# Kernel optimization log

Measured on AMD Instinct MI355X. Metric: run time of the kernel, lower is better.

Reference implementation:

```python
import jax, jax.numpy as jnp
import numpy as np

EPS = 1e-5  # torch LayerNorm default eps
ALIBI_SLOPE = 1.0

def layer_norm(x, g, b):
    mu = x.mean(-1, keepdims=True)
    var = ((x - mu) ** 2).mean(-1, keepdims=True)
    return (x - mu) * jax.lax.rsqrt(var + EPS) * g + b

def setup_inputs() -> dict:
    key = jax.random.key(0)
    B, T, D, DK, F = 4, 4096, 1024, 128, 2048  # F = ffn_mult * d_model
    ks = jax.random.split(key, 6)
    def s(k, shp, fan):
        return jax.random.normal(k, shp, jnp.float32) / np.sqrt(fan).astype(np.float32)
    return {
        'x': jax.random.normal(ks[0], (B, T, D), jnp.float32),
        'ln1_g': jnp.ones((D,), jnp.float32), 'ln1_b': jnp.zeros((D,), jnp.float32),
        'Wq': s(ks[1], (DK, D), D),  # torch Linear weight layout (out, in)
        'Wk': s(ks[2], (DK, D), D),
        'Wv': s(ks[3], (D, D), D),
        'ln2_g': jnp.ones((D,), jnp.float32), 'ln2_b': jnp.zeros((D,), jnp.float32),
        'W1': s(ks[4], (F, D), D), 'b1': jnp.zeros((F,), jnp.float32),
        'W2': s(ks[5], (D, F), F), 'b2': jnp.zeros((D,), jnp.float32),
    }

def reference(x, ln1_g, ln1_b, Wq, Wk, Wv, ln2_g, ln2_b, W1, b1, W2, b2):
    B, T, D = x.shape
    dk = Wq.shape[0]
    h = layer_norm(x, ln1_g, ln1_b)
    q = jnp.einsum('btd,kd->btk', h, Wq)
    k = jnp.einsum('btd,kd->btk', h, Wk)
    att = jnp.einsum('btk,bsk->bts', q, k) * (dk ** -0.5)  # [B,T,T]
    pos = jnp.arange(T)
    dist = jnp.clip(pos[:, None] - pos[None, :], 0).astype(att.dtype)
    att = att - ALIBI_SLOPE * dist  # alibi bias
    causal = pos[:, None] >= pos[None, :]
    att = jnp.where(causal, att, -jnp.inf)
    att = jax.nn.softmax(att, axis=-1)
    ctx = jnp.einsum('bts,bsd->btd', att, h)  # note: attends over h, not a v-projection
    x = x + jnp.einsum('btd,ed->bte', ctx, Wv)
    h2 = layer_norm(x, ln2_g, ln2_b)
    ff = jnp.maximum(jnp.einsum('btd,fd->btf', h2, W1) + b1, 0.0)
    x = x + jnp.einsum('btf,df->btd', ff, W2) + b2
    return x
```

## Files before the change

kernel.cpp:

```cpp
#include <hip/hip_runtime.h>
#include <stdint.h>

typedef __attribute__((ext_vector_type(4))) float f32x4;
typedef __attribute__((ext_vector_type(8))) unsigned short u16x8;
typedef __attribute__((ext_vector_type(4))) unsigned short u16x4;
typedef unsigned short bf16_t;

#define DEV __device__ __forceinline__

DEV void mfma16(f32x4& d, u16x8 a, u16x8 b) {
    asm("v_mfma_f32_16x16x32_bf16 %0, %1, %2, %0" : "+v"(d) : "v"(a), "v"(b));
}

DEV bf16_t f2bf(float f) {
    uint32_t u = __builtin_bit_cast(uint32_t, f);
    return (bf16_t)((u + 0x7fffu + ((u >> 16) & 1u)) >> 16);
}

DEV void async_g2l16(const void* g, void* l) {
    __builtin_amdgcn_global_load_lds(
        (const __attribute__((address_space(1))) uint32_t*)(uintptr_t)g,
        (__attribute__((address_space(3))) uint32_t*)(uint32_t)(uintptr_t)l,
        16, 0, 0);
}

DEV void blockbar() {
    asm volatile("" ::: "memory");
    __builtin_amdgcn_s_barrier();
    asm volatile("" ::: "memory");
}

#define VMCNT(n) asm volatile("s_waitcnt vmcnt(" #n ")" ::: "memory")

template <int EPI>
__global__ __launch_bounds__(512, 4) void gemm256x128_nt(
    const bf16_t* __restrict__ A, const bf16_t* __restrict__ B,
    void* __restrict__ Cp, const float* __restrict__ bias,
    const float* __restrict__ res, int M, int N, int K)
{
    __shared__ bf16_t sA[2 * 8192];
    __shared__ bf16_t sB[2 * 4096];
    const int tid = threadIdx.x;
    const int wave = tid >> 6, lane = tid & 63;
    const int lcol = lane & 15, krow = lane >> 4;
    const int wm = wave >> 1, wn = wave & 1;

    int id  = blockIdx.y * gridDim.x + blockIdx.x;
    int nwg = gridDim.x * gridDim.y;
    int swz = ((nwg & 7) == 0) ? ((id & 7) * (nwg >> 3) + (id >> 3)) : id;
    const int bn = swz % gridDim.y;
    const int bm = swz / gridDim.y;
    const int row_a = bm * 256, col_c = bn * 128;

    const int tq = tid >> 2;
    const int tr = (((tid & 3) ^ ((tid >> 3) & 3)) * 8);
    const bf16_t* aSt = A + (size_t)(row_a + tq) * K + tr;
    const bf16_t* bSt = B + (size_t)(col_c + tq) * K + tr;
    const size_t rowstep = (size_t)128 * K;
    bf16_t* ldsAw = sA + wave * 512;
    bf16_t* ldsBw = sB + wave * 512;

    const int cswz = (krow ^ ((lcol >> 1) & 3)) * 8;
    const int raOff = (wm * 64 + lcol) * 32 + cswz;
    const int rbOff = (wn * 64 + lcol) * 32 + cswz;

    f32x4 acc[4][4] = {};
    const int nt = K >> 5;

    async_g2l16(aSt,           ldsAw);
    async_g2l16(aSt + rowstep, ldsAw + 4096);
    async_g2l16(bSt,           ldsBw);
    VMCNT(0);
    blockbar();

    for (int t = 0; t < nt; ++t) {
        const int ra = (t & 1) ? 8192 : 0;
        const int rb = (t & 1) ? 4096 : 0;
        const int wa = 8192 - ra, wb = 4096 - rb;
        const bool pf = (t + 1) < nt;
        const size_t ko = (size_t)(t + 1) * 32;
        u16x8 fa[4], fb[4];
#pragma unroll
        for (int i = 0; i < 4; i++) fa[i] = *(const u16x8*)&sA[ra + raOff + i * 512];
#pragma unroll
        for (int i = 0; i < 4; i++) fb[i] = *(const u16x8*)&sB[rb + rbOff + i * 512];
        if (pf) {
            async_g2l16(aSt + ko,           ldsAw + wa);
            async_g2l16(aSt + ko + rowstep, ldsAw + wa + 4096);
            async_g2l16(bSt + ko,           ldsBw + wb);
        }
        __builtin_amdgcn_s_setprio(1);
#pragma unroll
        for (int mi = 0; mi < 4; mi++)
#pragma unroll
            for (int ni = 0; ni < 4; ni++)
                mfma16(acc[mi][ni], fa[mi], fb[ni]);
        __builtin_amdgcn_s_setprio(0);
        VMCNT(0);
        blockbar();
    }

#pragma unroll
    for (int mi = 0; mi < 4; mi++)
#pragma unroll
        for (int ni = 0; ni < 4; ni++)
#pragma unroll
            for (int j = 0; j < 4; j++) {
                const int gr = row_a + wm * 64 + mi * 16 + krow * 4 + j;
                const int gc = col_c + wn * 64 + ni * 16 + lcol;
                float v = acc[mi][ni][j];
                if (EPI == 0) {
                    ((bf16_t*)Cp)[(size_t)gr * N + gc] = f2bf(v);
                } else if (EPI == 1) {
                    v += bias[gc];
                    v = fmaxf(v, 0.f);
                    ((bf16_t*)Cp)[(size_t)gr * N + gc] = f2bf(v);
                } else if (EPI == 2) {
                    ((float*)Cp)[(size_t)gr * N + gc] = v + res[(size_t)gr * N + gc];
                } else {
                    ((float*)Cp)[(size_t)gr * N + gc] = v + bias[gc] + res[(size_t)gr * N + gc];
                }
            }
}

template <int EPI>
__global__ __launch_bounds__(256) void gemm_nt(
    const bf16_t* __restrict__ A, const bf16_t* __restrict__ B,
    void* __restrict__ Cp, const float* __restrict__ bias,
    const float* __restrict__ res, int M, int N, int K)
{
    alignas(16) __shared__ bf16_t sA[128 * 32];
    alignas(16) __shared__ bf16_t sB[128 * 32];
    const int tid = threadIdx.x;
    const int wave = tid >> 6, lane = tid & 63;
    const int lcol = lane & 15, krow = lane >> 4;

    int id  = blockIdx.y * gridDim.x + blockIdx.x;
    int nwg = gridDim.x * gridDim.y;
    int swz = ((nwg & 7) == 0) ? ((id & 7) * (nwg >> 3) + (id >> 3)) : id;
    const int bn = swz % gridDim.y;
    const int bm = swz / gridDim.y;

    const int row_a = bm * 128, col_c = bn * 128;
    const int wm = (wave >> 1) * 64, wn = (wave & 1) * 64;

    const int   srow  = wave * 16 + (lane >> 2);
    const int   scol  = (lane & 3) * 8;
    const bf16_t* aSrc = A + (size_t)(row_a + srow) * K + scol;
    const bf16_t* bSrc = B + (size_t)(col_c + srow) * K + scol;
    char* sAl = (char*)sA + wave * 1024;
    char* sBl = (char*)sB + wave * 1024;
    const size_t rstep = (size_t)64 * K;

    f32x4 acc[4][4] = {};

    for (int k0 = 0; k0 < K; k0 += 32) {
        async_g2l16(aSrc + k0,         sAl);
        async_g2l16(aSrc + k0 + rstep, sAl + 4096);
        async_g2l16(bSrc + k0,         sBl);
        async_g2l16(bSrc + k0 + rstep, sBl + 4096);
        __syncthreads();
        u16x8 af[4], bfr[4];
#pragma unroll
        for (int i = 0; i < 4; i++) {
            af[i]  = *(const u16x8*)&sA[(wm + i * 16 + lcol) * 32 + krow * 8];
            bfr[i] = *(const u16x8*)&sB[(wn + i * 16 + lcol) * 32 + krow * 8];
        }
#pragma unroll
        for (int mi = 0; mi < 4; mi++)
#pragma unroll
            for (int ni = 0; ni < 4; ni++)
                mfma16(acc[mi][ni], af[mi], bfr[ni]);
        __syncthreads();
    }

#pragma unroll
    for (int mi = 0; mi < 4; mi++)
#pragma unroll
        for (int ni = 0; ni < 4; ni++)
#pragma unroll
            for (int j = 0; j < 4; j++) {
                const int gr = row_a + wm + mi * 16 + krow * 4 + j;
                const int gc = col_c + wn + ni * 16 + lcol;
                float v = acc[mi][ni][j];
                if (EPI == 0) {
                    ((bf16_t*)Cp)[(size_t)gr * N + gc] = f2bf(v);
                } else if (EPI == 1) {
                    v += bias[gc];
                    v = fmaxf(v, 0.f);
                    ((bf16_t*)Cp)[(size_t)gr * N + gc] = f2bf(v);
                } else if (EPI == 2) {
                    ((float*)Cp)[(size_t)gr * N + gc] = v + res[(size_t)gr * N + gc];
                } else {
                    ((float*)Cp)[(size_t)gr * N + gc] = v + bias[gc] + res[(size_t)gr * N + gc];
                }
            }
}

__global__ __launch_bounds__(256) void ln_kernel(
    const float* __restrict__ X, const float* __restrict__ G,
    const float* __restrict__ Bt, bf16_t* __restrict__ O)
{
    const int row = blockIdx.x, tid = threadIdx.x;
    const int wave = tid >> 6, lane = tid & 63;
    const size_t base = (size_t)row * 1024 + tid * 4;
    f32x4 xv = *(const f32x4*)&X[base];
    float s  = xv[0] + xv[1] + xv[2] + xv[3];
    float s2 = xv[0]*xv[0] + xv[1]*xv[1] + xv[2]*xv[2] + xv[3]*xv[3];
#pragma unroll
    for (int o = 1; o < 64; o <<= 1) { s += __shfl_xor(s, o); s2 += __shfl_xor(s2, o); }
    __shared__ float red[8];
    if (lane == 0) { red[wave] = s; red[wave + 4] = s2; }
    __syncthreads();
    s  = red[0] + red[1] + red[2] + red[3];
    s2 = red[4] + red[5] + red[6] + red[7];
    const float mu = s * (1.f / 1024.f);
    const float rs = rsqrtf(s2 * (1.f / 1024.f) - mu * mu + 1e-5f);
    f32x4 gv = *(const f32x4*)&G[tid * 4];
    f32x4 bv = *(const f32x4*)&Bt[tid * 4];
    u16x4 ov;
#pragma unroll
    for (int i = 0; i < 4; i++) ov[i] = f2bf((xv[i] - mu) * rs * gv[i] + bv[i]);
    *(u16x4*)&O[base] = ov;
}

__global__ __launch_bounds__(256) void cvt_f32_bf16(
    const float* __restrict__ src, bf16_t* __restrict__ dst, int n)
{
    int i = (blockIdx.x * 256 + threadIdx.x) * 4;
    if (i >= n) return;
    f32x4 v = *(const f32x4*)&src[i];
    u16x4 o;
#pragma unroll
    for (int t = 0; t < 4; t++) o[t] = f2bf(v[t]);
    *(u16x4*)&dst[i] = o;
}

__global__ __launch_bounds__(256) void attn_p(
    const bf16_t* __restrict__ QK, bf16_t* __restrict__ P, int T)
{
    const int tid = threadIdx.x, w = tid >> 6, lane = tid & 63;
    const int lcol = lane & 15, krow = lane >> 4;
    const int qt = blockIdx.x;
    const int ntb = T >> 6;
    const int b = qt / ntb;
    const int r0 = (qt - b * ntb) << 6;
    const size_t g0 = (size_t)b * T + r0;
    const int jbase = r0 - 192;
    const float scale = 0.08838834764831845f;

    __shared__ float lred[2][4][64];

    u16x8 qf[4][4];
#pragma unroll
    for (int mf = 0; mf < 4; mf++)
#pragma unroll
        for (int ks = 0; ks < 4; ks++)
            qf[mf][ks] = *(const u16x8*)&QK[(g0 + mf * 16 + lcol) * 256 + ks * 32 + krow * 8];

    f32x4 acc[4][4] = {};
    const size_t kbase = (size_t)b * T * 256 + 128;
#pragma unroll
    for (int ks = 0; ks < 4; ks++) {
        u16x8 kf[4];
#pragma unroll
        for (int nf = 0; nf < 4; nf++) {
            int jc = jbase + w * 64 + nf * 16 + lcol;
            int jr = jc < 0 ? 0 : jc;
            kf[nf] = *(const u16x8*)&QK[kbase + (size_t)jr * 256 + ks * 32 + krow * 8];
        }
#pragma unroll
        for (int mf = 0; mf < 4; mf++)
#pragma unroll
            for (int nf = 0; nf < 4; nf++)
                mfma16(acc[mf][nf], qf[mf][ks], kf[nf]);
    }

#pragma unroll
    for (int mf = 0; mf < 4; mf++)
#pragma unroll
        for (int j = 0; j < 4; j++) {
            const int i_ = r0 + mf * 16 + krow * 4 + j;
            float m = -1e30f;
#pragma unroll
            for (int nf = 0; nf < 4; nf++) {
                const int jc = jbase + w * 64 + nf * 16 + lcol;
                float sv = (jc >= 0 && jc <= i_) ? acc[mf][nf][j] * scale - (float)(i_ - jc) : -1e30f;
                acc[mf][nf][j] = sv;
                m = fmaxf(m, sv);
            }
#pragma unroll
            for (int o = 1; o < 16; o <<= 1) m = fmaxf(m, __shfl_xor(m, o));
            if (lcol == 0) lred[0][w][mf * 16 + krow * 4 + j] = m;
        }
    __syncthreads();

#pragma unroll
    for (int mf = 0; mf < 4; mf++)
#pragma unroll
        for (int j = 0; j < 4; j++) {
            const int rr = mf * 16 + krow * 4 + j;
            const float m = fmaxf(fmaxf(lred[0][0][rr], lred[0][1][rr]),
                                  fmaxf(lred[0][2][rr], lred[0][3][rr]));
            float sm = 0.f;
#pragma unroll
            for (int nf = 0; nf < 4; nf++) {
                float p = __expf(acc[mf][nf][j] - m);
                acc[mf][nf][j] = p;
                sm += p;
            }
#pragma unroll
            for (int o = 1; o < 16; o <<= 1) sm += __shfl_xor(sm, o);
            if (lcol == 0) lred[1][w][rr] = sm;
        }
    __syncthreads();

    float inv_l[4][4];
#pragma unroll
    for (int mf = 0; mf < 4; mf++)
#pragma unroll
        for (int j = 0; j < 4; j++) {
            const int rr = mf * 16 + krow * 4 + j;
            inv_l[mf][j] = 1.f / (lred[1][0][rr] + lred[1][1][rr] + lred[1][2][rr] + lred[1][3][rr]);
        }
#pragma unroll
    for (int mf = 0; mf < 4; mf++)
#pragma unroll
        for (int nf = 0; nf < 4; nf++)
#pragma unroll
            for (int j = 0; j < 4; j++) {
                const int rr = mf * 16 + krow * 4 + j;
                P[((size_t)qt * 64 + rr) * 256 + w * 64 + nf * 16 + lcol] =
                    f2bf(acc[mf][nf][j] * inv_l[mf][j]);
            }
}

__global__ __launch_bounds__(256) void pv_gemm(
    const bf16_t* __restrict__ P, const bf16_t* __restrict__ H,
    bf16_t* __restrict__ CTX, int T)
{
    alignas(16) __shared__ bf16_t sHt[128 * 40];
    const int tid = threadIdx.x, w = tid >> 6, lane = tid & 63;
    const int lcol = lane & 15, krow = lane >> 4;
    const int qt = blockIdx.x, d0 = blockIdx.y * 128;
    const int ntb = T >> 6, b = qt / ntb;
    const int r0 = (qt - b * ntb) << 6;
    const int jbase = r0 - 192;
    const int wm = (w >> 1) * 32, wn = (w & 1) * 64;
    const int kk = tid >> 3, seg = tid & 7;

    f32x4 acc[2][4] = {};
    for (int k0 = 0; k0 < 256; k0 += 32) {
        int j = jbase + k0 + kk;
        if (j < 0) j = 0;
        const bf16_t* hp = H + ((size_t)b * T + j) * 1024 + d0 + seg * 16;
        u16x8 v0 = *(const u16x8*)hp;
        u16x8 v1 = *(const u16x8*)(hp + 8);
        __syncthreads();
#pragma unroll
        for (int i = 0; i < 8; i++) {
            sHt[(seg * 16 + i) * 40 + kk]     = v0[i];
            sHt[(seg * 16 + 8 + i) * 40 + kk] = v1[i];
        }
        __syncthreads();
        u16x8 af[2], bfr[4];
#pragma unroll
        for (int mi = 0; mi < 2; mi++)
            af[mi] = *(const u16x8*)&P[((size_t)qt * 64 + wm + mi * 16 + lcol) * 256 + k0 + krow * 8];
#pragma unroll
        for (int ni = 0; ni < 4; ni++)
            bfr[ni] = *(const u16x8*)&sHt[(wn + ni * 16 + lcol) * 40 + krow * 8];
#pragma unroll
        for (int mi = 0; mi < 2; mi++)
#pragma unroll
            for (int ni = 0; ni < 4; ni++)
                mfma16(acc[mi][ni], af[mi], bfr[ni]);
    }
#pragma unroll
    for (int mi = 0; mi < 2; mi++)
#pragma unroll
        for (int ni = 0; ni < 4; ni++)
#pragma unroll
            for (int j = 0; j < 4; j++)
                CTX[((size_t)b * T + r0 + wm + mi * 16 + krow * 4 + j) * 1024 +
                    d0 + wn + ni * 16 + lcol] = f2bf(acc[mi][ni][j]);
}

extern "C" void kernel_launch(void* const* d_in, const int* in_sizes, int n_in,
                              void* d_out, int out_size, void* d_ws, size_t ws_size,
                              hipStream_t stream)
{
    const float* x   = (const float*)d_in[0];
    const float* g1  = (const float*)d_in[1];
    const float* be1 = (const float*)d_in[2];
    const float* Wq  = (const float*)d_in[3];
    const float* Wk  = (const float*)d_in[4];
    const float* Wv  = (const float*)d_in[5];
    const float* g2  = (const float*)d_in[6];
    const float* be2 = (const float*)d_in[7];
    const float* W1  = (const float*)d_in[8];
    const float* b1  = (const float*)d_in[9];
    const float* W2  = (const float*)d_in[10];
    const float* b2  = (const float*)d_in[11];

    const int B = 4, T = 4096, D = 1024, DK = 128, F = 2048;
    const int BT = B * T;

    char* ws = (char*)d_ws;
    size_t off = 0;
    auto alloc = [&](size_t bytes) {
        void* p = ws + off;
        off += (bytes + 255) & ~(size_t)255;
        return p;
    };
    bf16_t* wqk_b = (bf16_t*)alloc((size_t)2 * DK * D * 2);
    bf16_t* wv_b  = (bf16_t*)alloc((size_t)D * D * 2);
    bf16_t* w1_b  = (bf16_t*)alloc((size_t)F * D * 2);
    bf16_t* w2_b  = (bf16_t*)alloc((size_t)D * F * 2);
    bf16_t* h     = (bf16_t*)alloc((size_t)BT * D * 2);
    bf16_t* qk    = (bf16_t*)alloc((size_t)BT * 256 * 2);
    bf16_t* P     = (bf16_t*)alloc((size_t)BT * 256 * 2);
    bf16_t* ctx   = (bf16_t*)alloc((size_t)BT * D * 2);
    bf16_t* ff    = (bf16_t*)alloc((size_t)BT * F * 2);
    if (ws_size < off) return;
    float* x2 = (float*)d_out;

    cvt_f32_bf16<<<DK * D / 1024, 256, 0, stream>>>(Wq, wqk_b, DK * D);
    cvt_f32_bf16<<<DK * D / 1024, 256, 0, stream>>>(Wk, wqk_b + (size_t)DK * D, DK * D);
    cvt_f32_bf16<<<D * D / 1024, 256, 0, stream>>>(Wv, wv_b, D * D);
    cvt_f32_bf16<<<F * D / 1024, 256, 0, stream>>>(W1, w1_b, F * D);
    cvt_f32_bf16<<<D * F / 1024, 256, 0, stream>>>(W2, w2_b, D * F);

    ln_kernel<<<BT, 256, 0, stream>>>(x, g1, be1, h);

    gemm_nt<0><<<dim3(BT / 128, 2), 256, 0, stream>>>(h, wqk_b, qk, nullptr, nullptr, BT, 256, D);

    attn_p<<<BT / 64, 256, 0, stream>>>(qk, P, T);
    pv_gemm<<<dim3(BT / 64, D / 128), 256, 0, stream>>>(P, h, ctx, T);

    gemm256x128_nt<2><<<dim3(BT / 256, D / 128), 512, 0, stream>>>(ctx, wv_b, x2, nullptr, x, BT, D, D);

    ln_kernel<<<BT, 256, 0, stream>>>(x2, g2, be2, h);

    gemm256x128_nt<1><<<dim3(BT / 256, F / 128), 512, 0, stream>>>(h, w1_b, ff, b1, nullptr, BT, F, D);

    gemm256x128_nt<3><<<dim3(BT / 256, D / 128), 512, 0, stream>>>(ff, w2_b, x2, b2, x2, BT, D, F);
}
```

Before: 360.4 us.

## Enlarge dense GEMM tiles to 256x256 with 64-wide K steps

The dense GEMMs (Wv projection, W1, W2) move from a 256x128 tile with K-step 32 to a 256x256 tile with K-step 64. Waves are rearranged 2x4, and each wave now computes a 128x64 sub-tile using 8x4 accumulators. The aim is higher arithmetic intensity per LDS and global load and fewer barriers per FLOP. The cost is twice the LDS (128KB double-buffered), higher register pressure and occupancy lowered to 2 blocks. It also leaves fewer workgroups (e.g. 256 for the D-output GEMMs), which may underfill 256 CUs.

```diff
diff --git a/kernel.cpp b/kernel.cpp
--- a/kernel.cpp
+++ b/kernel.cpp
@@ -33,80 +33,96 @@
 #define VMCNT(n) asm volatile("s_waitcnt vmcnt(" #n ")" ::: "memory")
 
 template <int EPI>
-__global__ __launch_bounds__(512, 4) void gemm256x128_nt(
+__global__ __launch_bounds__(512, 2) void gemm256_nt(
     const bf16_t* __restrict__ A, const bf16_t* __restrict__ B,
     void* __restrict__ Cp, const float* __restrict__ bias,
     const float* __restrict__ res, int M, int N, int K)
 {
-    __shared__ bf16_t sA[2 * 8192];
-    __shared__ bf16_t sB[2 * 4096];
+    __shared__ bf16_t sA[2 * 16384];
+    __shared__ bf16_t sB[2 * 16384];
     const int tid = threadIdx.x;
     const int wave = tid >> 6, lane = tid & 63;
     const int lcol = lane & 15, krow = lane >> 4;
-    const int wm = wave >> 1, wn = wave & 1;
+    const int wm = wave >> 2, wn = wave & 3;
 
     int id  = blockIdx.y * gridDim.x + blockIdx.x;
     int nwg = gridDim.x * gridDim.y;
     int swz = ((nwg & 7) == 0) ? ((id & 7) * (nwg >> 3) + (id >> 3)) : id;
     const int bn = swz % gridDim.y;
     const int bm = swz / gridDim.y;
-    const int row_a = bm * 256, col_c = bn * 128;
-
-    const int tq = tid >> 2;
-    const int tr = (((tid & 3) ^ ((tid >> 3) & 3)) * 8);
-    const bf16_t* aSt = A + (size_t)(row_a + tq) * K + tr;
-    const bf16_t* bSt = B + (size_t)(col_c + tq) * K + tr;
-    const size_t rowstep = (size_t)128 * K;
+    const int row_a = bm * 256, col_c = bn * 256;
+
+    const int trow = tid >> 3;
+    const int tr = (((tid & 7) ^ ((tid >> 3) & 7)) * 8);
+    const bf16_t* aSt = A + (size_t)(row_a + trow) * K + tr;
+    const bf16_t* bSt = B + (size_t)(col_c + trow) * K + tr;
+    const size_t rstep = (size_t)64 * K;
     bf16_t* ldsAw = sA + wave * 512;
     bf16_t* ldsBw = sB + wave * 512;
 
-    const int cswz = (krow ^ ((lcol >> 1) & 3)) * 8;
-    const int raOff = (wm * 64 + lcol) * 32 + cswz;
-    const int rbOff = (wn * 64 + lcol) * 32 + cswz;
-
-    f32x4 acc[4][4] = {};
-    const int nt = K >> 5;
-
-    async_g2l16(aSt,           ldsAw);
-    async_g2l16(aSt + rowstep, ldsAw + 4096);
-    async_g2l16(bSt,           ldsBw);
+    const int rowA = wm * 128 + lcol;
+    const int rowB = wn * 64  + lcol;
+    const int cA0 = ((krow ^ (rowA & 7))) * 8;
+    const int cB0 = ((krow ^ (rowB & 7))) * 8;
+    const int aBase = rowA * 64 + cA0;
+    const int bBase = rowB * 64 + cB0;
+
+    f32x4 acc[8][4] = {};
+    const int nt = K >> 6;
+
+#pragma unroll
+    for (int i = 0; i < 4; i++) {
+        async_g2l16(aSt + (size_t)i * rstep, ldsAw + i * 4096);
+        async_g2l16(bSt + (size_t)i * rstep, ldsBw + i * 4096);
+    }
     VMCNT(0);
     blockbar();
 
     for (int t = 0; t < nt; ++t) {
-        const int ra = (t & 1) ? 8192 : 0;
-        const int rb = (t & 1) ? 4096 : 0;
-        const int wa = 8192 - ra, wb = 4096 - rb;
+        const int rbase = (t & 1) ? 16384 : 0;
+        const int wbase = 16384 - rbase;
         const bool pf = (t + 1) < nt;
-        const size_t ko = (size_t)(t + 1) * 32;
-        u16x8 fa[4], fb[4];
-#pragma unroll
-        for (int i = 0; i < 4; i++) fa[i] = *(const u16x8*)&sA[ra + raOff + i * 512];
-#pragma unroll
-        for (int i = 0; i < 4; i++) fb[i] = *(const u16x8*)&sB[rb + rbOff + i * 512];
+        const size_t ko = (size_t)(t + 1) * 64;
+
         if (pf) {
-            async_g2l16(aSt + ko,           ldsAw + wa);
-            async_g2l16(aSt + ko + rowstep, ldsAw + wa + 4096);
-            async_g2l16(bSt + ko,           ldsBw + wb);
-        }
-        __builtin_amdgcn_s_setprio(1);
-#pragma unroll
-        for (int mi = 0; mi < 4; mi++)
+#pragma unroll
+            for (int i = 0; i < 4; i++) {
+                async_g2l16(aSt + ko + (size_t)i * rstep, ldsAw + wbase + i * 4096);
+                async_g2l16(bSt + ko + (size_t)i * rstep, ldsBw + wbase + i * 4096);
+            }
+        }
+
+        u16x8 fa[8], fb[4];
+#pragma unroll
+        for (int mi = 0; mi < 8; mi++) fa[mi] = *(const u16x8*)&sA[rbase + aBase + mi * 1024];
+#pragma unroll
+        for (int ni = 0; ni < 4; ni++) fb[ni] = *(const u16x8*)&sB[rbase + bBase + ni * 1024];
+#pragma unroll
+        for (int mi = 0; mi < 8; mi++)
 #pragma unroll
             for (int ni = 0; ni < 4; ni++)
                 mfma16(acc[mi][ni], fa[mi], fb[ni]);
-        __builtin_amdgcn_s_setprio(0);
+#pragma unroll
+        for (int mi = 0; mi < 8; mi++) fa[mi] = *(const u16x8*)&sA[rbase + ((aBase + mi * 1024) ^ 32)];
+#pragma unroll
+        for (int ni = 0; ni < 4; ni++) fb[ni] = *(const u16x8*)&sB[rbase + ((bBase + ni * 1024) ^ 32)];
+#pragma unroll
+        for (int mi = 0; mi < 8; mi++)
+#pragma unroll
+            for (int ni = 0; ni < 4; ni++)
+                mfma16(acc[mi][ni], fa[mi], fb[ni]);
+
         VMCNT(0);
         blockbar();
     }
 
 #pragma unroll
-    for (int mi = 0; mi < 4; mi++)
+    for (int mi = 0; mi < 8; mi++)
 #pragma unroll
         for (int ni = 0; ni < 4; ni++)
 #pragma unroll
             for (int j = 0; j < 4; j++) {
-                const int gr = row_a + wm * 64 + mi * 16 + krow * 4 + j;
+                const int gr = row_a + wm * 128 + mi * 16 + krow * 4 + j;
                 const int gc = col_c + wn * 64 + ni * 16 + lcol;
                 float v = acc[mi][ni][j];
                 if (EPI == 0) {
@@ -438,11 +454,11 @@
     attn_p<<<BT / 64, 256, 0, stream>>>(qk, P, T);
     pv_gemm<<<dim3(BT / 64, D / 128), 256, 0, stream>>>(P, h, ctx, T);
 
-    gemm256x128_nt<2><<<dim3(BT / 256, D / 128), 512, 0, stream>>>(ctx, wv_b, x2, nullptr, x, BT, D, D);
+    gemm256_nt<2><<<dim3(BT / 256, D / 256), 512, 0, stream>>>(ctx, wv_b, x2, nullptr, x, BT, D, D);
 
     ln_kernel<<<BT, 256, 0, stream>>>(x2, g2, be2, h);
 
-    gemm256x128_nt<1><<<dim3(BT / 256, F / 128), 512, 0, stream>>>(h, w1_b, ff, b1, nullptr, BT, F, D);
-
-    gemm256x128_nt<3><<<dim3(BT / 256, D / 128), 512, 0, stream>>>(ff, w2_b, x2, b2, x2, BT, D, F);
-}
+    gemm256_nt<1><<<dim3(BT / 256, F / 256), 512, 0, stream>>>(h, w1_b, ff, b1, nullptr, BT, F, D);
+
+    gemm256_nt<3><<<dim3(BT / 256, D / 256), 512, 0, stream>>>(ff, w2_b, x2, b2, x2, BT, D, F);
+}
```

Result: faster. 336.0 us (-6.8%).
